# Performance work log

Measured on AMD Instinct MI355X. Metric: run time of the kernel, lower is better.

## Reference

```python
import jax, jax.numpy as jnp
import numpy as np

L, NH, H, V, MAXP = 12, 12, 768, 50257, 1024
HD = H // NH
EPS = 1e-5


def setup_inputs() -> dict:
    key = jax.random.key(0)
    ks = iter(jax.random.split(key, 32))
    s = 0.02
    inp = {
        "input_ids": jax.random.randint(next(ks), (8, 1024), 0, V),
        "tok_emb": jax.random.normal(next(ks), (V, H), jnp.float32) * s,
        "pos_emb": jax.random.normal(next(ks), (MAXP, H), jnp.float32) * s,
        "ln1_g": jnp.ones((L, H), jnp.float32),
        "ln1_b": jnp.zeros((L, H), jnp.float32),
        "w_attn": jax.random.normal(next(ks), (L, H, 3 * H), jnp.float32) * s,
        "b_attn": jnp.zeros((L, 3 * H), jnp.float32),
        "w_out": jax.random.normal(next(ks), (L, H, H), jnp.float32) * s,
        "b_out": jnp.zeros((L, H), jnp.float32),
        "ln2_g": jnp.ones((L, H), jnp.float32),
        "ln2_b": jnp.zeros((L, H), jnp.float32),
        "w1": jax.random.normal(next(ks), (L, H, 4 * H), jnp.float32) * s,
        "b1": jnp.zeros((L, 4 * H), jnp.float32),
        "w2": jax.random.normal(next(ks), (L, 4 * H, H), jnp.float32) * s,
        "b2": jnp.zeros((L, H), jnp.float32),
        "lnf_g": jnp.ones((H,), jnp.float32),
        "lnf_b": jnp.zeros((H,), jnp.float32),
    }
    return inp


def _ln(x, g, b):
    mu = jnp.mean(x, axis=-1, keepdims=True)
    var = jnp.var(x, axis=-1, keepdims=True)
    return (x - mu) * jax.lax.rsqrt(var + EPS) * g + b


def _gpt2_forward(input_ids, tok_emb, pos_emb, ln1_g, ln1_b, w_attn, b_attn,
                  w_out, b_out, ln2_g, ln2_b, w1, b1, w2, b2, lnf_g, lnf_b):
    B, S = input_ids.shape
    x = tok_emb[input_ids] + pos_emb[:S]  # [B,S,H]
    # causal mask: True above the diagonal (future positions)
    mask = jnp.triu(jnp.ones((S, S), dtype=bool), k=1)
    inv_sqrt_hd = 1.0 / np.sqrt(HD)
    for l in range(L):
        n1 = _ln(x, ln1_g[l], ln1_b[l])
        qkv = n1 @ w_attn[l] + b_attn[l]  # [B,S,3H]
        q, k, v = jnp.split(qkv, 3, axis=-1)
        q = q.reshape(B, S, NH, HD).transpose(0, 2, 1, 3)
        k = k.reshape(B, S, NH, HD).transpose(0, 2, 1, 3)
        v = v.reshape(B, S, NH, HD).transpose(0, 2, 1, 3)
        scores = jnp.einsum('bhtd,bhsd->bhts', q, k)  # [B,NH,S,S]
        # faithful to source: mask with -10000 BEFORE dividing by sqrt(head_size)
        scores = jnp.where(mask, -10000.0, scores) * inv_sqrt_hd
        probs = jax.nn.softmax(scores, axis=-1)
        attn = jnp.einsum('bhts,bhsd->bhtd', probs, v)
        attn = attn.transpose(0, 2, 1, 3).reshape(B, S, H)
        attn = attn @ w_out[l] + b_out[l]
        x = x + attn
        n2 = _ln(x, ln2_g[l], ln2_b[l])
        h = jax.nn.gelu(n2 @ w1[l] + b1[l], approximate=False)
        x = x + (h @ w2[l] + b2[l])
    x = _ln(x, lnf_g, lnf_b)
    final_encoding = x[:, -1]  # [B,H]
    logits = final_encoding @ tok_emb.T  # tied weights, [B,V]
    return logits, final_encoding


def reference(input_ids, tok_emb, pos_emb, ln1_g, ln1_b, w_attn, b_attn,
              w_out, b_out, ln2_g, ln2_b, w1, b1, w2, b2, lnf_g, lnf_b):
    return _gpt2_forward(input_ids, tok_emb, pos_emb, ln1_g, ln1_b, w_attn,
                         b_attn, w_out, b_out, ln2_g, ln2_b, w1, b1, w2, b2,
                         lnf_g, lnf_b)
```

## Files before the change

### kernel.cpp

```cpp
#include <hip/hip_runtime.h>
#include <cmath>

typedef unsigned short u16;
typedef __bf16 bf16;
typedef __attribute__((ext_vector_type(8))) bf16 bf16x8;
typedef __attribute__((ext_vector_type(4))) float f32x4;

#define DINL __device__ __forceinline__

#define BB 8
#define SS 1024
#define HH 768
#define LL 12
#define NHH 12
#define HDD 64
#define MM 8192
#define VV 50257

DINL u16 f2bf(float f) {
    unsigned int u = __builtin_bit_cast(unsigned int, f);
    u += 0x7fff + ((u >> 16) & 1);
    return (u16)(u >> 16);
}

DINL bf16x8 ld_bf8(const u16* p) { return *(const bf16x8*)p; }

typedef __attribute__((address_space(1))) unsigned int as1_u32;
typedef __attribute__((address_space(3))) unsigned int as3_u32;

DINL void gllds16(const void* g, void* l) {
    __builtin_amdgcn_global_load_lds((as1_u32*)g, (as3_u32*)l, 16, 0, 0);
}

#define BARRIER()                                   \
    do {                                            \
        asm volatile("" ::: "memory");              \
        __builtin_amdgcn_s_barrier();               \
        asm volatile("" ::: "memory");              \
    } while (0)

DINL void xcd_remap(int gx, int& mTile, int& nTile) {
    int i = blockIdx.y * gx + blockIdx.x;
    int xcd = i & 7, j = i >> 3;
    nTile = j % gx;
    mTile = (j / gx) * 8 + xcd;
}

__global__ __launch_bounds__(256) void k_embed(const int* __restrict__ ids,
                                               const float* __restrict__ tok,
                                               const float* __restrict__ pos,
                                               float* __restrict__ x) {
    int tk = blockIdx.x;
    int s = tk & (SS - 1);
    int id = ids[tk];
    const float* tr = tok + (size_t)id * HH;
    const float* pr = pos + (size_t)s * HH;
    float* xr = x + (size_t)tk * HH;
#pragma unroll
    for (int j = 0; j < 3; j++) {
        int d = threadIdx.x + j * 256;
        xr[d] = tr[d] + pr[d];
    }
}

__global__ __launch_bounds__(256) void k_tcvt(const float* __restrict__ src, u16* __restrict__ dst,
                                              int R, int C, size_t sstr, size_t dstr) {
    src += (size_t)blockIdx.z * sstr;
    dst += (size_t)blockIdx.z * dstr;
    __shared__ float t[32][33];
    int tx = threadIdx.x & 31, ty = threadIdx.x >> 5;
    int c0 = blockIdx.x * 32, r0 = blockIdx.y * 32;
#pragma unroll
    for (int p = 0; p < 4; p++)
        t[ty + p * 8][tx] = src[(size_t)(r0 + ty + p * 8) * C + c0 + tx];
    __syncthreads();
#pragma unroll
    for (int p = 0; p < 4; p++)
        dst[(size_t)(c0 + ty + p * 8) * R + r0 + tx] = f2bf(t[tx][ty + p * 8]);
}

template <bool F32OUT>
__global__ __launch_bounds__(256) void k_ln(const float* __restrict__ x, const float* __restrict__ g,
                                            const float* __restrict__ b, void* __restrict__ outp,
                                            int nrows, int rs, int ro) {
    int w = threadIdx.x >> 6, lane = threadIdx.x & 63;
    int row = blockIdx.x * 4 + w;
    if (row >= nrows) return;
    const float4* xr = (const float4*)(x + ((size_t)row * rs + ro) * HH);
    float4 v[3];
    float s = 0.f, s2 = 0.f;
#pragma unroll
    for (int j = 0; j < 3; j++) {
        v[j] = xr[lane + 64 * j];
        s += v[j].x + v[j].y + v[j].z + v[j].w;
        s2 += v[j].x * v[j].x + v[j].y * v[j].y + v[j].z * v[j].z + v[j].w * v[j].w;
    }
#pragma unroll
    for (int off = 32; off; off >>= 1) {
        s += __shfl_xor(s, off, 64);
        s2 += __shfl_xor(s2, off, 64);
    }
    float mu = s * (1.0f / HH);
    float rstd = rsqrtf(s2 * (1.0f / HH) - mu * mu + 1e-5f);
#pragma unroll
    for (int j = 0; j < 3; j++) {
        int d4 = lane + 64 * j;
        float4 gv = ((const float4*)g)[d4];
        float4 bv = ((const float4*)b)[d4];
        float o0 = (v[j].x - mu) * rstd * gv.x + bv.x;
        float o1 = (v[j].y - mu) * rstd * gv.y + bv.y;
        float o2 = (v[j].z - mu) * rstd * gv.z + bv.z;
        float o3 = (v[j].w - mu) * rstd * gv.w + bv.w;
        if (F32OUT) {
            ((float4*)outp)[(size_t)row * (HH / 4) + d4] = make_float4(o0, o1, o2, o3);
        } else {
            ushort4 pk;
            pk.x = f2bf(o0); pk.y = f2bf(o1); pk.z = f2bf(o2); pk.w = f2bf(o3);
            *(ushort4*)((u16*)outp + (size_t)row * HH + d4 * 4) = pk;
        }
    }
}

template <int EPI>
__global__ __launch_bounds__(512, 2) void k_gemm256(const u16* __restrict__ A, const u16* __restrict__ BT,
                                                    const float* __restrict__ bias,
                                                    u16* __restrict__ obuf, u16* __restrict__ qb,
                                                    u16* __restrict__ kb, u16* __restrict__ vb,
                                                    int N, int K) {
    extern __shared__ u16 LD[];
    const int t = threadIdx.x, w = t >> 6, lane = t & 63;
    const int l15 = lane & 15, l4 = lane >> 4;
    const int wm = w >> 2, wn = w & 3;
    int mT, nT;
    xcd_remap(gridDim.x, mT, nT);
    const int m0 = mT * 256, n0 = nT * 256;
    const int KT = K >> 6, NI = KT >> 1;

    auto seg = [&](int buf, int mat, int h) -> u16* {
        return LD + (size_t)(((buf * 2 + mat) * 2 + h) * 8192);
    };

    auto stageH = [&](int buf, int mat, int h, int kt) {
        const u16* src = mat ? BT : A;
        const int base0 = mat ? n0 : m0;
        u16* dst = seg(buf, mat, h);
#pragma unroll
        for (int i = 0; i < 2; i++) {
            int rl = w * 16 + i * 8 + (lane >> 3);
            int c = lane & 7;
            int sc = (c ^ (rl & 7)) * 8;
            gllds16(src + (size_t)(base0 + h * 128 + rl) * K + kt * 64 + sc,
                    dst + (w * 16 + i * 8) * 64);
        }
    };

    f32x4 acc[8][4] = {};
    const int csw = l15 & 7;

    auto rdA = [&](int buf, int mh, bf16x8 a[4][2]) {
        const u16* p = seg(buf, 0, wm);
#pragma unroll
        for (int f = 0; f < 4; f++)
#pragma unroll
            for (int s = 0; s < 2; s++)
                a[f][s] = ld_bf8(p + (mh * 64 + f * 16 + l15) * 64 + ((s * 4 + l4) ^ csw) * 8);
    };
    auto rdB = [&](int buf, bf16x8 b[4][2]) {
        const u16* p = seg(buf, 1, wn >> 1);
#pragma unroll
        for (int f = 0; f < 4; f++)
#pragma unroll
            for (int s = 0; s < 2; s++)
                b[f][s] = ld_bf8(p + ((wn & 1) * 64 + f * 16 + l15) * 64 + ((s * 4 + l4) ^ csw) * 8);
    };

    stageH(0, 0, 0, 0); stageH(0, 0, 1, 0);
    stageH(0, 1, 0, 0); stageH(0, 1, 1, 0);
    stageH(1, 1, 0, 1); stageH(1, 1, 1, 1);
    asm volatile("s_waitcnt vmcnt(4)" ::: "memory");
    BARRIER();

    for (int i = 0; i < NI; ++i) {
        const int tE = 2 * i, tO = 2 * i + 1;
        const bool lst = (i == NI - 1);
        bf16x8 a[4][2], b[4][2];

        rdA(0, 0, a); rdB(0, b);
        stageH(1, 0, 0, tO); stageH(1, 0, 1, tO);
        __builtin_amdgcn_s_setprio(1);
#pragma unroll
        for (int f = 0; f < 4; f++)
#pragma unroll
            for (int nf = 0; nf < 4; nf++)
#pragma unroll
                for (int s = 0; s < 2; s++)
                    acc[f][nf] = __builtin_amdgcn_mfma_f32_16x16x32_bf16(a[f][s], b[nf][s], acc[f][nf], 0, 0, 0);
        __builtin_amdgcn_s_setprio(0);
        BARRIER();

        rdA(0, 1, a);
        if (!lst) { stageH(0, 1, 0, tE + 2); stageH(0, 1, 1, tE + 2); }
        __builtin_amdgcn_s_setprio(1);
#pragma unroll
        for (int f = 0; f < 4; f++)
#pragma unroll
            for (int nf = 0; nf < 4; nf++)
#pragma unroll
                for (int s = 0; s < 2; s++)
                    acc[4 + f][nf] = __builtin_amdgcn_mfma_f32_16x16x32_bf16(a[f][s], b[nf][s], acc[4 + f][nf], 0, 0, 0);
        __builtin_amdgcn_s_setprio(0);
        if (lst) asm volatile("s_waitcnt vmcnt(0)" ::: "memory");
        else     asm volatile("s_waitcnt vmcnt(4)" ::: "memory");
        BARRIER();

        rdA(1, 0, a); rdB(1, b);
        if (!lst) { stageH(0, 0, 0, tE + 2); stageH(0, 0, 1, tE + 2); }
        __builtin_amdgcn_s_setprio(1);
#pragma unroll
        for (int f = 0; f < 4; f++)
#pragma unroll
            for (int nf = 0; nf < 4; nf++)
#pragma unroll
                for (int s = 0; s < 2; s++)
                    acc[f][nf] = __builtin_amdgcn_mfma_f32_16x16x32_bf16(a[f][s], b[nf][s], acc[f][nf], 0, 0, 0);
        __builtin_amdgcn_s_setprio(0);
        BARRIER();

        rdA(1, 1, a);
        if (!lst) { stageH(1, 1, 0, tO + 2); stageH(1, 1, 1, tO + 2); }
        __builtin_amdgcn_s_setprio(1);
#pragma unroll
        for (int f = 0; f < 4; f++)
#pragma unroll
            for (int nf = 0; nf < 4; nf++)
#pragma unroll
                for (int s = 0; s < 2; s++)
                    acc[4 + f][nf] = __builtin_amdgcn_mfma_f32_16x16x32_bf16(a[f][s], b[nf][s], acc[4 + f][nf], 0, 0, 0);
        __builtin_amdgcn_s_setprio(0);
        if (!lst) asm volatile("s_waitcnt vmcnt(4)" ::: "memory");
        BARRIER();
    }

#pragma unroll
    for (int mf = 0; mf < 8; mf++) {
#pragma unroll
        for (int nf = 0; nf < 4; nf++) {
#pragma unroll
            for (int r = 0; r < 4; r++) {
                int row = m0 + wm * 128 + mf * 16 + l4 * 4 + r;
                int n = n0 + wn * 64 + nf * 16 + l15;
                float v = acc[mf][nf][r] + bias[n];
                if (EPI == 0) {
                    int sg = n / HH, wi = n % HH;
                    int h = wi >> 6, d = wi & 63;
                    int bi = row >> 10, s = row & (SS - 1);
                    size_t bh = (size_t)(bi * NHH + h);
                    if (sg == 0)
                        qb[(bh * SS + s) * HDD + d] = f2bf(v * 0.125f);
                    else if (sg == 1)
                        kb[(bh * SS + s) * HDD + d] = f2bf(v);
                    else
                        vb[(bh * HDD + d) * SS + s] = f2bf(v);
                } else {
                    float gl = 0.5f * v * (1.0f + erff(v * 0.70710678118654752f));
                    obuf[(size_t)row * N + n] = f2bf(gl);
                }
            }
        }
    }
}

__global__ __launch_bounds__(256) void k_gemm64(const u16* __restrict__ A, const u16* __restrict__ BT,
                                                const float* __restrict__ bias, float* __restrict__ xio,
                                                int N, int K) {
    __shared__ u16 As[2][128 * 32];
    __shared__ u16 Bs[2][64 * 32];
    const int t = threadIdx.x, w = t >> 6, lane = t & 63;
    const int l15 = lane & 15, l4 = lane >> 4;
    const int wr = w >> 1, wc = w & 1;
    int mT, nT;
    xcd_remap(gridDim.x, mT, nT);
    const int m0 = mT * 128, n0 = nT * 64;
    const int KT = K >> 5;

    f32x4 acc[4][2] = {};

    auto stage = [&](int buf, int kt) {
        int rr = lane >> 2;
        int kc = kt * 32 + (((lane & 3) ^ ((lane >> 3) & 3)) * 8);
#pragma unroll
        for (int i = 0; i < 2; i++) {
            int idx = w * 2 + i;
            gllds16(A + (size_t)(m0 + idx * 16 + rr) * K + kc, &As[buf][idx * 512]);
        }
        gllds16(BT + (size_t)(n0 + w * 16 + rr) * K + kc, &Bs[buf][w * 512]);
    };

    stage(0, 0);
    __syncthreads();
    int buf = 0;
    const int sw = (l15 >> 1) & 3;
    for (int kt = 0; kt < KT; ++kt) {
        if (kt + 1 < KT) stage(buf ^ 1, kt + 1);
        bf16x8 af[4], bfr[2];
#pragma unroll
        for (int i = 0; i < 4; i++) af[i] = ld_bf8(&As[buf][(wr * 64 + i * 16 + l15) * 32 + ((l4 ^ sw) * 8)]);
#pragma unroll
        for (int j = 0; j < 2; j++) bfr[j] = ld_bf8(&Bs[buf][(wc * 32 + j * 16 + l15) * 32 + ((l4 ^ sw) * 8)]);
#pragma unroll
        for (int i = 0; i < 4; i++)
#pragma unroll
            for (int j = 0; j < 2; j++)
                acc[i][j] = __builtin_amdgcn_mfma_f32_16x16x32_bf16(af[i], bfr[j], acc[i][j], 0, 0, 0);
        __syncthreads();
        buf ^= 1;
    }

#pragma unroll
    for (int i = 0; i < 4; i++) {
#pragma unroll
        for (int j = 0; j < 2; j++) {
#pragma unroll
            for (int r = 0; r < 4; r++) {
                int row = m0 + wr * 64 + i * 16 + l4 * 4 + r;
                int n = n0 + wc * 32 + j * 16 + l15;
                xio[(size_t)row * N + n] += acc[i][j][r] + bias[n];
            }
        }
    }
}

__global__ __launch_bounds__(256) void k_attn(const u16* __restrict__ q, const u16* __restrict__ k,
                                              const u16* __restrict__ vt, u16* __restrict__ o) {
    int qt = 15 - blockIdx.x;
    int bh = blockIdx.y;
    int w = threadIdx.x >> 6, lane = threadIdx.x & 63;
    int l15 = lane & 15, l4 = lane >> 4;

    __shared__ u16 Ks[2][64 * 64];
    __shared__ u16 Vs[2][64 * 64];
    __shared__ u16 pl[4][16 * 72];
    u16* pw = pl[w];

    const size_t bhq = (size_t)bh * SS * HDD;
    int qrow0 = qt * 64 + w * 16;

    auto stage = [&](int buf, int kvb) {
#pragma unroll
        for (int i = 0; i < 2; i++) {
            int rl = w * 16 + i * 8 + (lane >> 3);
            int c = lane & 7;
            int sc = (c ^ (rl & 7)) * 8;
            gllds16(k + bhq + (size_t)(kvb * 64 + rl) * HDD + sc, &Ks[buf][(w * 16 + i * 8) * 64]);
            gllds16(vt + ((size_t)bh * HDD + rl) * SS + kvb * 64 + sc, &Vs[buf][(w * 16 + i * 8) * 64]);
        }
    };

    bf16x8 aq[2];
#pragma unroll
    for (int ks = 0; ks < 2; ks++)
        aq[ks] = ld_bf8(q + bhq + (size_t)(qrow0 + l15) * HDD + ks * 32 + l4 * 8);

    f32x4 acc[4] = {};
    float mrun[4], psum[4];
#pragma unroll
    for (int r = 0; r < 4; r++) { mrun[r] = -1e30f; psum[r] = 0.f; }

    stage(0, 0);
    __syncthreads();
    int buf = 0;

    for (int kvb = 0; kvb <= qt; ++kvb) {
        if (kvb < qt) stage(buf ^ 1, kvb + 1);

        f32x4 s[4] = {};
#pragma unroll
        for (int c = 0; c < 4; c++) {
#pragma unroll
            for (int ks = 0; ks < 2; ks++) {
                bf16x8 kf = ld_bf8(&Ks[buf][(c * 16 + l15) * 64 + ((ks * 4 + l4) ^ (l15 & 7)) * 8]);
                s[c] = __builtin_amdgcn_mfma_f32_16x16x32_bf16(aq[ks], kf, s[c], 0, 0, 0);
            }
        }
        if (kvb == qt) {
#pragma unroll
            for (int c = 0; c < 4; c++) {
                int kvi = kvb * 64 + c * 16 + l15;
#pragma unroll
                for (int r = 0; r < 4; r++) {
                    int qi = qrow0 + l4 * 4 + r;
                    if (kvi > qi) s[c][r] = -1250.0f;
                }
            }
        }
        float lmax[4];
        int ok = 1;
#pragma unroll
        for (int r = 0; r < 4; r++) {
            lmax[r] = fmaxf(fmaxf(s[0][r], s[1][r]), fmaxf(s[2][r], s[3][r]));
            ok &= (lmax[r] <= mrun[r] + 8.f) ? 1 : 0;
        }
        if (!__all(ok)) {
#pragma unroll
            for (int off = 1; off < 16; off <<= 1)
#pragma unroll
                for (int r = 0; r < 4; r++) lmax[r] = fmaxf(lmax[r], __shfl_xor(lmax[r], off, 64));
#pragma unroll
            for (int r = 0; r < 4; r++) {
                float mnew = fmaxf(mrun[r], lmax[r]);
                float ef = __expf(mrun[r] - mnew);
                mrun[r] = mnew;
                psum[r] *= ef;
#pragma unroll
                for (int cd = 0; cd < 4; cd++) acc[cd][r] *= ef;
            }
        }
#pragma unroll
        for (int c = 0; c < 4; c++)
#pragma unroll
            for (int r = 0; r < 4; r++) {
                float pv = __expf(s[c][r] - mrun[r]);
                psum[r] += pv;
                pw[(l4 * 4 + r) * 72 + c * 16 + l15] = f2bf(pv);
            }
#pragma unroll
        for (int ks = 0; ks < 2; ks++) {
            bf16x8 pa = ld_bf8(pw + l15 * 72 + ks * 32 + l4 * 8);
#pragma unroll
            for (int cd = 0; cd < 4; cd++) {
                bf16x8 vf = ld_bf8(&Vs[buf][(cd * 16 + l15) * 64 + ((ks * 4 + l4) ^ (l15 & 7)) * 8]);
                acc[cd] = __builtin_amdgcn_mfma_f32_16x16x32_bf16(pa, vf, acc[cd], 0, 0, 0);
            }
        }
        __syncthreads();
        buf ^= 1;
    }

#pragma unroll
    for (int off = 1; off < 16; off <<= 1)
#pragma unroll
        for (int r = 0; r < 4; r++) psum[r] += __shfl_xor(psum[r], off, 64);

    int b = bh / NHH, h = bh % NHH;
#pragma unroll
    for (int cd = 0; cd < 4; cd++) {
#pragma unroll
        for (int r = 0; r < 4; r++) {
            int qi = qrow0 + l4 * 4 + r;
            float ov = acc[cd][r] / psum[r];
            o[((size_t)b * SS + qi) * HH + h * HDD + cd * 16 + l15] = f2bf(ov);
        }
    }
}

__global__ __launch_bounds__(256) void k_logits(const float* __restrict__ enc,
                                                const float* __restrict__ tok,
                                                float* __restrict__ out) {
    int w = threadIdx.x >> 6, lane = threadIdx.x & 63;
    int v = blockIdx.x * 4 + w;
    if (v >= VV) return;
    const float4* tr = (const float4*)(tok + (size_t)v * HH);
    float a[8];
#pragma unroll
    for (int b = 0; b < 8; b++) a[b] = 0.f;
#pragma unroll
    for (int j = 0; j < 3; j++) {
        float4 t4 = tr[lane + 64 * j];
#pragma unroll
        for (int b = 0; b < 8; b++) {
            float4 e4 = *(const float4*)(enc + (size_t)b * HH + (lane + 64 * j) * 4);
            a[b] += t4.x * e4.x + t4.y * e4.y + t4.z * e4.z + t4.w * e4.w;
        }
    }
#pragma unroll
    for (int off = 32; off; off >>= 1)
#pragma unroll
        for (int b = 0; b < 8; b++) a[b] += __shfl_xor(a[b], off, 64);
    if (lane == 0) {
#pragma unroll
        for (int b = 0; b < 8; b++) out[(size_t)b * VV + v] = a[b];
    }
}

extern "C" void kernel_launch(void* const* d_in, const int* in_sizes, int n_in,
                              void* d_out, int out_size, void* d_ws, size_t ws_size,
                              hipStream_t stream) {
    const int* ids = (const int*)d_in[0];
    const float* tok = (const float*)d_in[1];
    const float* pos = (const float*)d_in[2];
    const float* ln1g = (const float*)d_in[3];
    const float* ln1b = (const float*)d_in[4];
    const float* wat = (const float*)d_in[5];
    const float* bat = (const float*)d_in[6];
    const float* wou = (const float*)d_in[7];
    const float* bou = (const float*)d_in[8];
    const float* ln2g = (const float*)d_in[9];
    const float* ln2b = (const float*)d_in[10];
    const float* w1 = (const float*)d_in[11];
    const float* b1 = (const float*)d_in[12];
    const float* w2 = (const float*)d_in[13];
    const float* b2 = (const float*)d_in[14];
    const float* lnfg = (const float*)d_in[15];
    const float* lnfb = (const float*)d_in[16];

    char* ws = (char*)d_ws;
    float* xw = (float*)(ws + 0);
    u16* nb = (u16*)(ws + 25165824);
    u16* qb = (u16*)(ws + 37748736);
    u16* kb = (u16*)(ws + 50331648);
    u16* vb = (u16*)(ws + 62914560);
    u16* ab = (u16*)(ws + 75497472);
    u16* hb = (u16*)(ws + 88080384);
    u16* wt = (u16*)(ws + 138412032);
    const size_t LSTR = 7077888;
    const size_t WAO = 0, WOO = 1769472, W1O = 2359296, W2O = 4718592;

    float* outf = (float*)d_out;
    float* enc = outf + (size_t)BB * VV;

    static bool attrDone = false;
    if (!attrDone) {
        hipFuncSetAttribute(reinterpret_cast<const void*>(&k_gemm256<0>),
                            hipFuncAttributeMaxDynamicSharedMemorySize, 131072);
        hipFuncSetAttribute(reinterpret_cast<const void*>(&k_gemm256<2>),
                            hipFuncAttributeMaxDynamicSharedMemorySize, 131072);
        attrDone = true;
    }

    k_embed<<<MM, 256, 0, stream>>>(ids, tok, pos, xw);
    k_tcvt<<<dim3(72, 24, 12), 256, 0, stream>>>(wat, wt + WAO, 768, 2304, (size_t)768 * 2304, LSTR);
    k_tcvt<<<dim3(24, 24, 12), 256, 0, stream>>>(wou, wt + WOO, 768, 768, (size_t)768 * 768, LSTR);
    k_tcvt<<<dim3(96, 24, 12), 256, 0, stream>>>(w1, wt + W1O, 768, 3072, (size_t)768 * 3072, LSTR);
    k_tcvt<<<dim3(24, 96, 12), 256, 0, stream>>>(w2, wt + W2O, 3072, 768, (size_t)3072 * 768, LSTR);

    for (int l = 0; l < LL; l++) {
        const u16* wl = wt + (size_t)l * LSTR;
        k_ln<false><<<MM / 4, 256, 0, stream>>>(xw, ln1g + l * HH, ln1b + l * HH, nb, MM, 1, 0);
        k_gemm256<0><<<dim3(9, 32), 512, 131072, stream>>>(nb, wl + WAO, bat + (size_t)l * 2304,
                                                           nullptr, qb, kb, vb, 2304, 768);
        k_attn<<<dim3(16, 96), 256, 0, stream>>>(qb, kb, vb, ab);
        k_gemm64<<<dim3(12, 64), 256, 0, stream>>>(ab, wl + WOO, bou + (size_t)l * HH, xw, 768, 768);
        k_ln<false><<<MM / 4, 256, 0, stream>>>(xw, ln2g + l * HH, ln2b + l * HH, nb, MM, 1, 0);
        k_gemm256<2><<<dim3(12, 32), 512, 131072, stream>>>(nb, wl + W1O, b1 + (size_t)l * 3072,
                                                            hb, nullptr, nullptr, nullptr, 3072, 768);
        k_gemm64<<<dim3(12, 64), 256, 0, stream>>>(hb, wl + W2O, b2 + (size_t)l * HH, xw, 768, 3072);
    }
    k_ln<true><<<2, 256, 0, stream>>>(xw, lnfg, lnfb, enc, BB, SS, SS - 1);
    k_logits<<<(VV + 3) / 4, 256, 0, stream>>>(enc, tok, outf);
}
```

Before: 4.065 ms.

## Triple-buffer k_gemm64 with BK=64 tiles and explicit vmcnt waits

Reworks the N=768 residual GEMM so each K step covers 64 elements instead of 32, over three LDS stages prefetched two steps ahead. Global-to-LDS loads are fenced with explicit s_waitcnt vmcnt counts instead of a full __syncthreads after each step. It also adds an XOR swizzle over 8 chunks and raises wave priority around the MFMA block. The intent is to hide global load latency and halve the loop and barrier overhead, at the cost of more shared memory (72 KB) and possibly lower occupancy.

```diff
diff --git a/kernel.cpp b/kernel.cpp
--- a/kernel.cpp
+++ b/kernel.cpp
@@ -273,47 +273,73 @@
 __global__ __launch_bounds__(256) void k_gemm64(const u16* __restrict__ A, const u16* __restrict__ BT,
                                                 const float* __restrict__ bias, float* __restrict__ xio,
                                                 int N, int K) {
-    __shared__ u16 As[2][128 * 32];
-    __shared__ u16 Bs[2][64 * 32];
+    __shared__ u16 As[3][128 * 64];
+    __shared__ u16 Bs[3][64 * 64];
     const int t = threadIdx.x, w = t >> 6, lane = t & 63;
     const int l15 = lane & 15, l4 = lane >> 4;
     const int wr = w >> 1, wc = w & 1;
     int mT, nT;
     xcd_remap(gridDim.x, mT, nT);
     const int m0 = mT * 128, n0 = nT * 64;
-    const int KT = K >> 5;
+    const int KT = K >> 6;
 
     f32x4 acc[4][2] = {};
 
     auto stage = [&](int buf, int kt) {
-        int rr = lane >> 2;
-        int kc = kt * 32 + (((lane & 3) ^ ((lane >> 3) & 3)) * 8);
+        int rsub = lane >> 3;
+        int sc = ((lane & 7) ^ rsub) * 8;
+        int kc = kt * 64 + sc;
+#pragma unroll
+        for (int i = 0; i < 4; i++) {
+            int r0 = w * 32 + i * 8;
+            gllds16(A + (size_t)(m0 + r0 + rsub) * K + kc, &As[buf][r0 * 64]);
+        }
 #pragma unroll
         for (int i = 0; i < 2; i++) {
-            int idx = w * 2 + i;
-            gllds16(A + (size_t)(m0 + idx * 16 + rr) * K + kc, &As[buf][idx * 512]);
-        }
-        gllds16(BT + (size_t)(n0 + w * 16 + rr) * K + kc, &Bs[buf][w * 512]);
+            int r0 = w * 16 + i * 8;
+            gllds16(BT + (size_t)(n0 + r0 + rsub) * K + kc, &Bs[buf][r0 * 64]);
+        }
     };
 
     stage(0, 0);
-    __syncthreads();
-    int buf = 0;
-    const int sw = (l15 >> 1) & 3;
+    if (KT > 1) stage(1, 1);
+    const int csw = l15 & 7;
+
     for (int kt = 0; kt < KT; ++kt) {
-        if (kt + 1 < KT) stage(buf ^ 1, kt + 1);
-        bf16x8 af[4], bfr[2];
-#pragma unroll
-        for (int i = 0; i < 4; i++) af[i] = ld_bf8(&As[buf][(wr * 64 + i * 16 + l15) * 32 + ((l4 ^ sw) * 8)]);
-#pragma unroll
-        for (int j = 0; j < 2; j++) bfr[j] = ld_bf8(&Bs[buf][(wc * 32 + j * 16 + l15) * 32 + ((l4 ^ sw) * 8)]);
+        int nb = kt + 2;
+        if (nb < KT) {
+            stage(nb % 3, nb);
+            asm volatile("s_waitcnt vmcnt(12)" ::: "memory");
+        } else if (kt + 1 < KT) {
+            asm volatile("s_waitcnt vmcnt(6)" ::: "memory");
+        } else {
+            asm volatile("s_waitcnt vmcnt(0)" ::: "memory");
+        }
+        BARRIER();
+
+        const u16* ap = As[kt % 3];
+        const u16* bp = Bs[kt % 3];
+        bf16x8 af[4][2], bf2[2][2];
 #pragma unroll
         for (int i = 0; i < 4; i++)
 #pragma unroll
+            for (int s = 0; s < 2; s++)
+                af[i][s] = ld_bf8(ap + (wr * 64 + i * 16 + l15) * 64 + ((s * 4 + l4) ^ csw) * 8);
+#pragma unroll
+        for (int j = 0; j < 2; j++)
+#pragma unroll
+            for (int s = 0; s < 2; s++)
+                bf2[j][s] = ld_bf8(bp + (wc * 32 + j * 16 + l15) * 64 + ((s * 4 + l4) ^ csw) * 8);
+        __builtin_amdgcn_s_setprio(1);
+#pragma unroll
+        for (int i = 0; i < 4; i++)
+#pragma unroll
             for (int j = 0; j < 2; j++)
-                acc[i][j] = __builtin_amdgcn_mfma_f32_16x16x32_bf16(af[i], bfr[j], acc[i][j], 0, 0, 0);
-        __syncthreads();
-        buf ^= 1;
+#pragma unroll
+                for (int s = 0; s < 2; s++)
+                    acc[i][j] = __builtin_amdgcn_mfma_f32_16x16x32_bf16(af[i][s], bf2[j][s], acc[i][j], 0, 0, 0);
+        __builtin_amdgcn_s_setprio(0);
+        BARRIER();
     }
 
 #pragma unroll
```

Result: slower. 4.476 ms (+10.1%).
